# Kernel optimization log

Hardware: AMD Instinct MI355X
Metric: run time of the kernel (lower is better)

Reference implementation:

```python
import jax, jax.numpy as jnp
import numpy as np

T, B, C, HF, H, W, E, TOP_K = 4, 32, 384, 1536, 14, 14, 8, 2
AUX_W = 0.01
ALPHA = 2.0  # spikingjelly ATan surrogate default

@jax.custom_vjp
def spike(v):
    return (v >= 0.0).astype(v.dtype)

def _spike_fwd(v):
    return spike(v), v

def _spike_bwd(v, g):
    sg = (ALPHA / 2.0) / (1.0 + (jnp.pi / 2.0 * ALPHA * v) ** 2)
    return (g * sg,)

spike.defvjp(_spike_fwd, _spike_bwd)

def lif_multistep(x, tau):
    # x: (T, ...). decay_input=True, v_threshold=1, hard reset to 0, detach_reset
    def step(v, xt):
        v = v + (xt - v) / tau
        s = spike(v - 1.0)
        v = v * (1.0 - jax.lax.stop_gradient(s))
        return v, s
    _, s = jax.lax.scan(step, jnp.zeros_like(x[0]), x)
    return s

def bn_eval(y, gamma, beta, mean, var, eps=1e-5):
    inv = gamma / jnp.sqrt(var + eps)
    return y * inv[None, :, None, None] + (beta - mean * inv)[None, :, None, None]

def setup_inputs() -> dict:
    key = jax.random.key(0)
    ks = jax.random.split(key, 8)
    d = {"x": jax.random.normal(ks[0], (T, B, C, H, W), jnp.float32)}
    d["rw"] = jax.random.normal(ks[1], (E, C), jnp.float32) * 0.02
    d["rb"] = jnp.zeros((E,), jnp.float32)
    d["r_gamma"] = jnp.ones((E,), jnp.float32)
    d["r_beta"] = jnp.zeros((E,), jnp.float32)
    d["r_mean"] = jax.random.normal(ks[2], (E,), jnp.float32) * 0.01
    d["r_var"] = jax.random.uniform(ks[3], (E,), jnp.float32, 0.75, 1.25)
    d["w1"] = jax.random.normal(ks[4], (E, HF, C), jnp.float32) * 0.02
    d["b1"] = jnp.zeros((E, HF), jnp.float32)
    d["g1"] = jnp.ones((E, HF), jnp.float32)
    d["be1"] = jnp.zeros((E, HF), jnp.float32)
    d["m1"] = jax.random.normal(ks[5], (E, HF), jnp.float32) * 0.01
    d["v1"] = jnp.ones((E, HF), jnp.float32)
    d["w2"] = jax.random.normal(ks[6], (E, C, HF), jnp.float32) * 0.02
    d["b2"] = jnp.zeros((E, C), jnp.float32)
    d["g2"] = jnp.ones((E, C), jnp.float32)
    d["be2"] = jnp.zeros((E, C), jnp.float32)
    d["m2"] = jax.random.normal(ks[7], (E, C), jnp.float32) * 0.01
    d["v2"] = jnp.ones((E, C), jnp.float32)
    d["taus"] = jnp.linspace(1.5, 4.0, E, dtype=jnp.float32)
    return d

def reference(x, rw, rb, r_gamma, r_beta, r_mean, r_var,
              w1, b1, g1, be1, m1, v1, w2, b2, g2, be2, m2, v2, taus):
    Tn, Bn, Cn, Hn, Wn = x.shape
    N = Tn * Bn
    # ---- SpikeRouter ----
    s = lif_multistep(x, 2.0)                                   # (T,B,C,H,W)
    r = jnp.einsum('tbchw,ec->tbehw', s, rw) + rb[None, None, :, None, None]
    r = bn_eval(r.reshape(N, E, Hn, Wn), r_gamma, r_beta, r_mean, r_var)
    logits = r.mean(axis=(-2, -1))                              # (N,E)
    probs = jax.nn.softmax(logits, axis=-1)
    tkw, tki = jax.lax.top_k(probs, TOP_K)
    tkw = tkw / tkw.sum(axis=-1, keepdims=True)
    one_hot = jax.nn.one_hot(tki, E, dtype=x.dtype)             # (N,K,E)
    gate = (one_hot * tkw[..., None]).sum(axis=1)               # (N,E), 0 for unselected
    # ---- expert dispatch/combine (dense, math-equivalent: gate==0 masks out) ----
    xt = x.reshape(N, Cn, Hn, Wn)
    out = jnp.zeros_like(xt)
    for e in range(E):
        s1 = spike(xt / taus[e] - 1.0)                          # T=1 LIF step
        h = jnp.einsum('nchw,oc->nohw', s1, w1[e]) + b1[e][None, :, None, None]
        h = bn_eval(h, g1[e], be1[e], m1[e], v1[e])
        s2 = spike(h / taus[e] - 1.0)
        o = jnp.einsum('nchw,oc->nohw', s2, w2[e]) + b2[e][None, :, None, None]
        o = bn_eval(o, g2[e], be2[e], m2[e], v2[e])
        o = o + xt                                              # final residual
        out = out + gate[:, e, None, None, None] * o
    # ---- Switch-style load balancing loss ----
    f = one_hot.sum(axis=1).mean(axis=0)                        # fraction routed per expert
    p = probs.mean(axis=0)
    aux = AUX_W * E * jnp.sum(f * p)
    return out.reshape(Tn, Bn, Cn, Hn, Wn), aux
```

## Files before the change

kernel.cpp:

```cpp
#include <hip/hip_runtime.h>
#include <hip/hip_bf16.h>
#include <cstdint>
#include <math.h>

#define T_  4
#define B_  32
#define C_  384
#define HF_ 1536
#define HW_ 196
#define E_  8
#define N_  128
#define REC_CAP 16384
#define NROW 1792
#define NGT  50176
#define LCAP 64

#define LIFB (B_ * C_)
#define TRB  (E_ * 12 * 24)
#define PRB  48

__global__ __launch_bounds__(256) void k_lifprep(
    const float* __restrict__ x, float* __restrict__ cnt,
    const float* __restrict__ w1, __hip_bfloat16* __restrict__ w1t,
    const float* b1, const float* g1, const float* be1,
    const float* m1, const float* v1,
    const float* b2, const float* g2, const float* be2,
    const float* m2, const float* v2,
    const float* taus,
    float* A, float* Bc, float* const2, float* inv2v,
    float* rowmaxp, int* header) {
  __shared__ float tile[64][33];
  __shared__ int c4[T_];
  int blk = blockIdx.x;
  int tid = threadIdx.x;

  if (blk < LIFB) {
    if (tid < T_) c4[tid] = 0;
    __syncthreads();
    int bc = blk;
    bool act = tid < HW_;
    float v = 0.f;
    size_t base = (size_t)bc * HW_ + (act ? tid : 0);
    #pragma unroll
    for (int t = 0; t < T_; ++t) {
      float xv = act ? x[base + (size_t)t * B_ * C_ * HW_] : -1e30f;
      v = v + (xv - v) * 0.5f;
      bool sp = (v - 1.0f >= 0.0f);
      if (sp) v = 0.f;
      unsigned long long m = __ballot(act && sp);
      if ((tid & 63) == 0) atomicAdd(&c4[t], __popcll(m));
    }
    __syncthreads();
    if (tid < T_) cnt[(size_t)tid * B_ * C_ + bc] = (float)c4[tid];
  } else if (blk < LIFB + TRB) {
    int rem = blk - LIFB;
    int e = rem / 288, r2 = rem % 288;
    int ct = r2 / 24, ot = r2 % 24;
    int c0 = ct * 32, o0 = ot * 64;
    int cl = tid & 31, olb = tid >> 5;
    #pragma unroll
    for (int it = 0; it < 8; ++it) {
      int ol = olb + it * 8;
      tile[ol][cl] = w1[(size_t)(e * HF_ + o0 + ol) * C_ + c0 + cl];
    }
    __syncthreads();
    int ol2 = tid & 63, clb = tid >> 6;
    #pragma unroll
    for (int it = 0; it < 8; ++it) {
      int cl2 = clb + it * 4;
      w1t[(size_t)(e * C_ + c0 + cl2) * HF_ + o0 + ol2] =
          __float2bfloat16(tile[ol2][cl2]);
    }
    if (tid < 32) {
      float m = 0.f;
      for (int ol = 0; ol < 64; ++ol) {
        float bv = __bfloat162float(__float2bfloat16(tile[ol][tid]));
        m = fmaxf(m, fabsf(bv));
      }
      rowmaxp[(size_t)(e * C_ + c0 + tid) * 24 + ot] = m;
    }
  } else {
    int idx = (blk - LIFB - TRB) * 256 + tid;
    if (idx < 64) header[idx] = 0;
    if (idx < E_ * HF_) {
      int e = idx / HF_;
      float inv = g1[idx] / sqrtf(v1[idx] + 1e-5f);
      float sh  = be1[idx] - m1[idx] * inv;
      A[idx]  = inv;
      Bc[idx] = inv * b1[idx] + sh - taus[e];
    }
    if (idx < E_ * C_) {
      float inv = g2[idx] / sqrtf(v2[idx] + 1e-5f);
      const2[idx] = b2[idx] * inv + (be2[idx] - m2[idx] * inv);
      inv2v[idx]  = inv;
    }
  }
}

__global__ __launch_bounds__(256) void k_router(
    const float* __restrict__ cnt, const float* __restrict__ rw,
    const float* rb, const float* rg, const float* rbeta,
    const float* rmean, const float* rvar,
    const float* __restrict__ const2,
    const float* __restrict__ rowmaxp, float* __restrict__ rowmax,
    const float* __restrict__ A, const float* __restrict__ Bc,
    float* __restrict__ thrmin,
    int* sel_e, float* sel_g, float* gsum, float* K,
    float* f_acc, float* p_acc) {
  __shared__ float sc[C_ + 256 + E_];
  __shared__ int s_i1, s_i2;
  __shared__ float s_g1, s_g2;
  int bid = blockIdx.x, tid = threadIdx.x;

  if (bid < N_) {
    int n = bid;
    float* part = sc + C_;
    float* lg = part + 256;
    for (int c = tid; c < C_; c += 256) sc[c] = cnt[(size_t)n * C_ + c];
    __syncthreads();
    {
      int e = tid >> 5, sub = tid & 31;
      float d = 0.f;
      for (int c = sub; c < C_; c += 32) d += rw[e * C_ + c] * sc[c];
      part[tid] = d;
    }
    __syncthreads();
    if (tid < E_) {
      float dot = 0.f;
      #pragma unroll
      for (int j = 0; j < 32; ++j) dot += part[tid * 32 + j];
      float inv = rg[tid] / sqrtf(rvar[tid] + 1e-5f);
      lg[tid] = (dot * (1.0f / HW_) + rb[tid]) * inv +
                (rbeta[tid] - rmean[tid] * inv);
    }
    __syncthreads();
    if (tid == 0) {
      float m = lg[0];
      for (int e = 1; e < E_; ++e) m = fmaxf(m, lg[e]);
      float pr[E_]; float s = 0.f;
      for (int e = 0; e < E_; ++e) { pr[e] = expf(lg[e] - m); s += pr[e]; }
      float invs = 1.0f / s;
      for (int e = 0; e < E_; ++e) pr[e] *= invs;
      int i1 = 0;
      for (int e = 1; e < E_; ++e) if (pr[e] > pr[i1]) i1 = e;
      int i2 = (i1 == 0) ? 1 : 0;
      for (int e = 0; e < E_; ++e) if (e != i1 && pr[e] > pr[i2]) i2 = e;
      float w = pr[i1] + pr[i2];
      float ga = pr[i1] / w, gb = pr[i2] / w;
      sel_e[2 * n] = i1; sel_e[2 * n + 1] = i2;
      sel_g[2 * n] = ga; sel_g[2 * n + 1] = gb;
      gsum[n] = ga + gb;
      s_i1 = i1; s_i2 = i2; s_g1 = ga; s_g2 = gb;
      atomicAdd(&f_acc[i1], 1.0f);
      atomicAdd(&f_acc[i2], 1.0f);
      for (int e = 0; e < E_; ++e) atomicAdd(&p_acc[e], pr[e]);
    }
    __syncthreads();
    int i1 = s_i1, i2 = s_i2; float ga = s_g1, gb = s_g2;
    for (int c = tid; c < C_; c += 256)
      K[(size_t)n * C_ + c] =
          ga * const2[i1 * C_ + c] + gb * const2[i2 * C_ + c];
  } else if (bid < N_ + 12) {
    int idx = (bid - N_) * 256 + tid;
    if (idx < E_ * C_) {
      float m = 0.f;
      #pragma unroll
      for (int t = 0; t < 24; ++t) m = fmaxf(m, rowmaxp[(size_t)idx * 24 + t]);
      rowmax[idx] = m;
    }
  } else {
    float* red = sc;
    for (int e = 0; e < E_; ++e) {
      float m = INFINITY;
      for (int o = tid; o < HF_; o += 256) {
        float a = A[e * HF_ + o], b = Bc[e * HF_ + o];
        float thr = (a != 0.0f) ? (-b / fabsf(a))
                                : ((b >= 0.0f) ? -INFINITY : INFINITY);
        m = fminf(m, thr);
      }
      red[tid] = m;
      __syncthreads();
      for (int s = 128; s > 0; s >>= 1) {
        if (tid < s) red[tid] = fminf(red[tid], red[tid + s]);
        __syncthreads();
      }
      if (tid == 0) thrmin[e] = red[0];
      __syncthreads();
    }
  }
}

__global__ __launch_bounds__(256) void k_lists(
    const float* __restrict__ x, const int* __restrict__ sel_e,
    const float* __restrict__ taus, const float* __restrict__ rowmax,
    const float* __restrict__ thrmin,
    const float* __restrict__ gsum, const float* __restrict__ K,
    float* __restrict__ out,
    int* __restrict__ nnzarr, unsigned short* __restrict__ list16) {
  __shared__ float xs[14 * 385];
  int bid = blockIdx.x, tid = threadIdx.x;
  int lane = tid & 63, wave = tid >> 6;
  int n = bid / 14, h = bid - n * 14;
  unsigned long long lmask = (1ull << lane) - 1ull;

  for (int idx = tid; idx < C_ * 7; idx += 256) {
    int c = idx / 7, wp = idx - c * 7;
    float2 v = *(const float2*)(x + ((size_t)(n * C_ + c) * 14 + h) * 14 + 2 * wp);
    xs[(2 * wp) * 385 + c]     = v.x;
    xs[(2 * wp + 1) * 385 + c] = v.y;
  }
  __syncthreads();

  for (int t = wave; t < 28; t += 4) {
    int k = t / 14, w = t - k * 14;
    int pair = 2 * n + k;
    int e = sel_e[pair];
    float tau = taus[e];
    const float* rme = rowmax + e * C_;
    int tw = pair * 196 + h * 14 + w;
    size_t lbase = (size_t)tw * LCAP;
    int nnz = 0;
    float myb = 0.f;
    #pragma unroll
    for (int cb = 0; cb < 6; ++cb) {
      int c = cb * 64 + lane;
      bool sp = (xs[w * 385 + c] / tau - 1.0f >= 0.0f);
      unsigned long long m = __ballot(sp);
      int pos = nnz + __popcll(m & lmask);
      if (sp) {
        if (pos < LCAP) list16[lbase + pos] = (unsigned short)c;
        myb += rme[c];
      }
      nnz += __popcll(m);
    }
    #pragma unroll
    for (int off = 1; off < 64; off <<= 1) myb += __shfl_xor(myb, off, 64);
    if (lane == 0) {
      bool prune = (myb < thrmin[e] - 1e-4f);
      nnzarr[tw] = prune ? -1 : (nnz < LCAP ? nnz : LCAP);
    }
  }

  float g = gsum[n];
  const float* Kn = K + (size_t)n * C_;
  for (int idx = tid; idx < C_ * 7; idx += 256) {
    int c = idx / 7, wp = idx - c * 7;
    float kc = Kn[c];
    float2 v;
    v.x = g * xs[(2 * wp) * 385 + c] + kc;
    v.y = g * xs[(2 * wp + 1) * 385 + c] + kc;
    *(float2*)(out + ((size_t)(n * C_ + c) * 14 + h) * 14 + 2 * wp) = v;
  }
}

__global__ __launch_bounds__(256, 4) void k_gather(
    const __hip_bfloat16* __restrict__ w1t,
    const float* __restrict__ A, const float* __restrict__ Bc,
    const int* __restrict__ sel_e,
    const int* __restrict__ nnzarr, const unsigned short* __restrict__ list16,
    int* __restrict__ rec, int* __restrict__ rec_count) {
  int tw = blockIdx.x * 4 + (threadIdx.x >> 6);
  int lane = threadIdx.x & 63;
  int nnz = nnzarr[tw];
  if (nnz < 0) return;
  int pair = tw / 196, pos = tw - pair * 196;
  int e = sel_e[pair];
  int lv = (int)list16[(size_t)tw * LCAP + lane];
  const uint4* wb = (const uint4*)(w1t + (size_t)e * C_ * HF_);

  #pragma unroll
  for (int pass = 0; pass < 3; ++pass) {
    const uint4* wbp = wb + pass * 64 + lane;
    float acc[8];
    #pragma unroll
    for (int q = 0; q < 8; ++q) acc[q] = 0.f;
    int j = 0;
    for (; j + 4 <= nnz; j += 4) {
      int c0 = __shfl(lv, j + 0);
      int c1 = __shfl(lv, j + 1);
      int c2 = __shfl(lv, j + 2);
      int c3 = __shfl(lv, j + 3);
      uint4 a = wbp[c0 * 192];
      uint4 b = wbp[c1 * 192];
      uint4 c = wbp[c2 * 192];
      uint4 d = wbp[c3 * 192];
      uint32_t ua[4] = {a.x, a.y, a.z, a.w};
      uint32_t ub[4] = {b.x, b.y, b.z, b.w};
      uint32_t uc[4] = {c.x, c.y, c.z, c.w};
      uint32_t ud[4] = {d.x, d.y, d.z, d.w};
      #pragma unroll
      for (int q = 0; q < 4; ++q) {
        acc[2 * q]     += __uint_as_float(ua[q] << 16) + __uint_as_float(ub[q] << 16) +
                          __uint_as_float(uc[q] << 16) + __uint_as_float(ud[q] << 16);
        acc[2 * q + 1] += __uint_as_float(ua[q] & 0xffff0000u) + __uint_as_float(ub[q] & 0xffff0000u) +
                          __uint_as_float(uc[q] & 0xffff0000u) + __uint_as_float(ud[q] & 0xffff0000u);
      }
    }
    for (; j < nnz; ++j) {
      int c0 = __shfl(lv, j);
      uint4 a = wbp[c0 * 192];
      uint32_t ua[4] = {a.x, a.y, a.z, a.w};
      #pragma unroll
      for (int q = 0; q < 4; ++q) {
        acc[2 * q]     += __uint_as_float(ua[q] << 16);
        acc[2 * q + 1] += __uint_as_float(ua[q] & 0xffff0000u);
      }
    }
    int k2 = (pass * 64 + lane) * 2;
    float4 Av0 = ((const float4*)(A + e * HF_))[k2];
    float4 Av1 = ((const float4*)(A + e * HF_))[k2 + 1];
    float4 Bv0 = ((const float4*)(Bc + e * HF_))[k2];
    float4 Bv1 = ((const float4*)(Bc + e * HF_))[k2 + 1];
    float av[8] = {Av0.x, Av0.y, Av0.z, Av0.w, Av1.x, Av1.y, Av1.z, Av1.w};
    float bv[8] = {Bv0.x, Bv0.y, Bv0.z, Bv0.w, Bv1.x, Bv1.y, Bv1.z, Bv1.w};
    #pragma unroll
    for (int q = 0; q < 8; ++q) {
      if (av[q] * acc[q] + bv[q] >= 0.0f) {
        int ridx = atomicAdd(rec_count, 1);
        if (ridx < REC_CAP) {
          rec[ridx * 3 + 0] = pair;
          rec[ridx * 3 + 1] = pos;
          rec[ridx * 3 + 2] = (pass * 64 + lane) * 8 + q;
        }
      }
    }
  }
}

__global__ void k_apply(const int* __restrict__ rec, const int* __restrict__ rec_count,
                        const int* __restrict__ sel_e, const float* __restrict__ sel_g,
                        const float* __restrict__ inv2v, const float* __restrict__ w2,
                        const float* f_acc, const float* p_acc,
                        float* __restrict__ out, float* aux_out) {
  int nrec = *rec_count;
  if (nrec > REC_CAP) nrec = REC_CAP;
  for (int r = blockIdx.x; r < nrec; r += gridDim.x) {
    int pair = rec[r * 3], pos = rec[r * 3 + 1], o = rec[r * 3 + 2];
    int n = pair >> 1;
    int e = sel_e[pair];
    float g = sel_g[pair];
    for (int c = threadIdx.x; c < C_; c += blockDim.x) {
      float wv = w2[(size_t)(e * C_ + c) * HF_ + o];
      atomicAdd(&out[(size_t)(n * C_ + c) * HW_ + pos],
                g * inv2v[e * C_ + c] * wv);
    }
  }
  if (blockIdx.x == 0 && threadIdx.x == 0) {
    float s = 0.f;
    for (int e = 0; e < E_; ++e)
      s += (f_acc[e] * (1.0f / N_)) * (p_acc[e] * (1.0f / N_));
    *aux_out = 0.01f * E_ * s;
  }
}

extern "C" void kernel_launch(void* const* d_in, const int* in_sizes, int n_in,
                              void* d_out, int out_size, void* d_ws, size_t ws_size,
                              hipStream_t stream) {
  const float* x       = (const float*)d_in[0];
  const float* rw      = (const float*)d_in[1];
  const float* rb      = (const float*)d_in[2];
  const float* r_gamma = (const float*)d_in[3];
  const float* r_beta  = (const float*)d_in[4];
  const float* r_mean  = (const float*)d_in[5];
  const float* r_var   = (const float*)d_in[6];
  const float* w1      = (const float*)d_in[7];
  const float* b1      = (const float*)d_in[8];
  const float* g1      = (const float*)d_in[9];
  const float* be1     = (const float*)d_in[10];
  const float* m1      = (const float*)d_in[11];
  const float* v1      = (const float*)d_in[12];
  const float* w2      = (const float*)d_in[13];
  const float* b2      = (const float*)d_in[14];
  const float* g2      = (const float*)d_in[15];
  const float* be2     = (const float*)d_in[16];
  const float* m2      = (const float*)d_in[17];
  const float* v2      = (const float*)d_in[18];
  const float* taus    = (const float*)d_in[19];
  float* out = (float*)d_out;

  char* ws = (char*)d_ws;
  int*   header = (int*)ws;
  float* f_acc  = (float*)ws + 8;
  float* p_acc  = (float*)ws + 16;
  float* cnt    = (float*)(ws + 256);
  int*   sel_e  = (int*)(ws + 196864);
  float* sel_g  = (float*)(ws + 197888);
  float* gsum   = (float*)(ws + 198912);
  float* K      = (float*)(ws + 199424);
  float* A      = (float*)(ws + 396032);
  float* Bc     = (float*)(ws + 445184);
  float* const2 = (float*)(ws + 494336);
  float* inv2v  = (float*)(ws + 506624);
  int*   rec    = (int*)(ws + 518912);
  __hip_bfloat16* w1t = (__hip_bfloat16*)(ws + 715520);
  int*   nnzarr = (int*)(ws + 10152704);
  unsigned short* list16 = (unsigned short*)(ws + 10353408);
  float* rowmaxp = (float*)(ws + 16775936);
  float* rowmax  = (float*)(ws + 17070848);
  float* thrmin  = (float*)(ws + 17083136);

  k_lifprep<<<LIFB + TRB + PRB, 256, 0, stream>>>(
      x, cnt, w1, w1t, b1, g1, be1, m1, v1, b2, g2, be2, m2, v2, taus,
      A, Bc, const2, inv2v, rowmaxp, header);
  k_router<<<N_ + 13, 256, 0, stream>>>(
      cnt, rw, rb, r_gamma, r_beta, r_mean, r_var, const2,
      rowmaxp, rowmax, A, Bc, thrmin,
      sel_e, sel_g, gsum, K, f_acc, p_acc);
  k_lists<<<NROW, 256, 0, stream>>>(
      x, sel_e, taus, rowmax, thrmin, gsum, K, out, nnzarr, list16);
  k_gather<<<NGT / 4, 256, 0, stream>>>(
      w1t, A, Bc, sel_e, nnzarr, list16, rec, header);
  k_apply<<<64, 256, 0, stream>>>(
      rec, header, sel_e, sel_g, inv2v, w2, f_acc, p_acc,
      out, out + (out_size - 1));
}
```

Before: 232.6 us.

## Compact unpruned tokens into a work queue and split combine into its own kernel

The list-building kernel now writes index lists only for positions that survive the pruning test, and appends each survivor to a compact queue through an atomic counter. The gather kernel runs a fixed grid of 2048 blocks as a persistent loop over that queue, so it no longer launches one wave per position only for most to exit early. The dense residual/gate write of the output moves into a separate vectorized float4 kernel. Risks: qcount (header+1) must be zeroed beforehand, presumably in lifprep as for the header. Queue order is nondeterministic, and the extra launch adds overhead.

```diff
diff --git a/kernel.cpp b/kernel.cpp
--- a/kernel.cpp
+++ b/kernel.cpp
@@ -194,9 +194,8 @@
     const float* __restrict__ x, const int* __restrict__ sel_e,
     const float* __restrict__ taus, const float* __restrict__ rowmax,
     const float* __restrict__ thrmin,
-    const float* __restrict__ gsum, const float* __restrict__ K,
-    float* __restrict__ out,
-    int* __restrict__ nnzarr, unsigned short* __restrict__ list16) {
+    unsigned short* __restrict__ list16,
+    int* __restrict__ queue, int* __restrict__ qcount) {
   __shared__ float xs[14 * 385];
   int bid = blockIdx.x, tid = threadIdx.x;
   int lane = tid & 63, wave = tid >> 6;
@@ -217,8 +216,7 @@
     int e = sel_e[pair];
     float tau = taus[e];
     const float* rme = rowmax + e * C_;
-    int tw = pair * 196 + h * 14 + w;
-    size_t lbase = (size_t)tw * LCAP;
+    unsigned long long masks[6];
     int nnz = 0;
     float myb = 0.f;
     #pragma unroll
@@ -226,101 +224,124 @@
       int c = cb * 64 + lane;
       bool sp = (xs[w * 385 + c] / tau - 1.0f >= 0.0f);
       unsigned long long m = __ballot(sp);
-      int pos = nnz + __popcll(m & lmask);
-      if (sp) {
-        if (pos < LCAP) list16[lbase + pos] = (unsigned short)c;
-        myb += rme[c];
-      }
+      masks[cb] = m;
+      if (sp) myb += rme[c];
       nnz += __popcll(m);
     }
     #pragma unroll
     for (int off = 1; off < 64; off <<= 1) myb += __shfl_xor(myb, off, 64);
-    if (lane == 0) {
-      bool prune = (myb < thrmin[e] - 1e-4f);
-      nnzarr[tw] = prune ? -1 : (nnz < LCAP ? nnz : LCAP);
-    }
-  }
-
-  float g = gsum[n];
-  const float* Kn = K + (size_t)n * C_;
-  for (int idx = tid; idx < C_ * 7; idx += 256) {
-    int c = idx / 7, wp = idx - c * 7;
-    float kc = Kn[c];
-    float2 v;
-    v.x = g * xs[(2 * wp) * 385 + c] + kc;
-    v.y = g * xs[(2 * wp + 1) * 385 + c] + kc;
-    *(float2*)(out + ((size_t)(n * C_ + c) * 14 + h) * 14 + 2 * wp) = v;
-  }
+    bool prune = (myb < thrmin[e] - 1e-4f);
+    if (!prune) {
+      int tw = pair * 196 + h * 14 + w;
+      size_t lbase = (size_t)tw * LCAP;
+      int cum = 0;
+      #pragma unroll
+      for (int cb = 0; cb < 6; ++cb) {
+        unsigned long long m = masks[cb];
+        bool sp = (m >> lane) & 1ull;
+        int pos = cum + __popcll(m & lmask);
+        if (sp && pos < LCAP) list16[lbase + pos] = (unsigned short)(cb * 64 + lane);
+        cum += __popcll(m);
+      }
+      if (lane == 0) {
+        int nv = nnz < LCAP ? nnz : LCAP;
+        int qi = atomicAdd(qcount, 1);
+        queue[qi] = tw | (nv << 20);
+      }
+    }
+  }
+}
+
+__global__ __launch_bounds__(256) void k_combine(
+    const float* __restrict__ x, const float* __restrict__ gsum,
+    const float* __restrict__ K, float* __restrict__ out) {
+  int idx = blockIdx.x * 256 + threadIdx.x;
+  int nc = idx / 49;
+  float g = gsum[nc / C_];
+  float kc = K[nc];
+  float4 v = ((const float4*)x)[idx];
+  v.x = g * v.x + kc;
+  v.y = g * v.y + kc;
+  v.z = g * v.z + kc;
+  v.w = g * v.w + kc;
+  ((float4*)out)[idx] = v;
 }
 
 __global__ __launch_bounds__(256, 4) void k_gather(
     const __hip_bfloat16* __restrict__ w1t,
     const float* __restrict__ A, const float* __restrict__ Bc,
     const int* __restrict__ sel_e,
-    const int* __restrict__ nnzarr, const unsigned short* __restrict__ list16,
+    const int* __restrict__ queue, const int* __restrict__ qcount,
+    const unsigned short* __restrict__ list16,
     int* __restrict__ rec, int* __restrict__ rec_count) {
-  int tw = blockIdx.x * 4 + (threadIdx.x >> 6);
+  int nq = *qcount;
+  int wid = blockIdx.x * 4 + (threadIdx.x >> 6);
   int lane = threadIdx.x & 63;
-  int nnz = nnzarr[tw];
-  if (nnz < 0) return;
-  int pair = tw / 196, pos = tw - pair * 196;
-  int e = sel_e[pair];
-  int lv = (int)list16[(size_t)tw * LCAP + lane];
-  const uint4* wb = (const uint4*)(w1t + (size_t)e * C_ * HF_);
-
-  #pragma unroll
-  for (int pass = 0; pass < 3; ++pass) {
-    const uint4* wbp = wb + pass * 64 + lane;
-    float acc[8];
-    #pragma unroll
-    for (int q = 0; q < 8; ++q) acc[q] = 0.f;
-    int j = 0;
-    for (; j + 4 <= nnz; j += 4) {
-      int c0 = __shfl(lv, j + 0);
-      int c1 = __shfl(lv, j + 1);
-      int c2 = __shfl(lv, j + 2);
-      int c3 = __shfl(lv, j + 3);
-      uint4 a = wbp[c0 * 192];
-      uint4 b = wbp[c1 * 192];
-      uint4 c = wbp[c2 * 192];
-      uint4 d = wbp[c3 * 192];
-      uint32_t ua[4] = {a.x, a.y, a.z, a.w};
-      uint32_t ub[4] = {b.x, b.y, b.z, b.w};
-      uint32_t uc[4] = {c.x, c.y, c.z, c.w};
-      uint32_t ud[4] = {d.x, d.y, d.z, d.w};
+  int nwaves = gridDim.x * 4;
+
+  for (int qi = wid; qi < nq; qi += nwaves) {
+    int ent = queue[qi];
+    int tw = ent & 0xFFFFF;
+    int nnz = ent >> 20;
+    int pair = tw / 196, pos = tw - pair * 196;
+    int e = sel_e[pair];
+    int lv = (int)list16[(size_t)tw * LCAP + lane];
+    const uint4* wb = (const uint4*)(w1t + (size_t)e * C_ * HF_);
+
+    #pragma unroll
+    for (int pass = 0; pass < 3; ++pass) {
+      const uint4* wbp = wb + pass * 64 + lane;
+      float acc[8];
       #pragma unroll
-      for (int q = 0; q < 4; ++q) {
-        acc[2 * q]     += __uint_as_float(ua[q] << 16) + __uint_as_float(ub[q] << 16) +
-                          __uint_as_float(uc[q] << 16) + __uint_as_float(ud[q] << 16);
-        acc[2 * q + 1] += __uint_as_float(ua[q] & 0xffff0000u) + __uint_as_float(ub[q] & 0xffff0000u) +
-                          __uint_as_float(uc[q] & 0xffff0000u) + __uint_as_float(ud[q] & 0xffff0000u);
-      }
-    }
-    for (; j < nnz; ++j) {
-      int c0 = __shfl(lv, j);
-      uint4 a = wbp[c0 * 192];
-      uint32_t ua[4] = {a.x, a.y, a.z, a.w};
+      for (int q = 0; q < 8; ++q) acc[q] = 0.f;
+      int j = 0;
+      for (; j + 4 <= nnz; j += 4) {
+        int c0 = __shfl(lv, j + 0);
+        int c1 = __shfl(lv, j + 1);
+        int c2 = __shfl(lv, j + 2);
+        int c3 = __shfl(lv, j + 3);
+        uint4 a = wbp[c0 * 192];
+        uint4 b = wbp[c1 * 192];
+        uint4 c = wbp[c2 * 192];
+        uint4 d = wbp[c3 * 192];
+        uint32_t ua[4] = {a.x, a.y, a.z, a.w};
+        uint32_t ub[4] = {b.x, b.y, b.z, b.w};
+        uint32_t uc[4] = {c.x, c.y, c.z, c.w};
+        uint32_t ud[4] = {d.x, d.y, d.z, d.w};
+        #pragma unroll
+        for (int q = 0; q < 4; ++q) {
+          acc[2 * q]     += __uint_as_float(ua[q] << 16) + __uint_as_float(ub[q] << 16) +
+                            __uint_as_float(uc[q] << 16) + __uint_as_float(ud[q] << 16);
+          acc[2 * q + 1] += __uint_as_float(ua[q] & 0xffff0000u) + __uint_as_float(ub[q] & 0xffff0000u) +
+                            __uint_as_float(uc[q] & 0xffff0000u) + __uint_as_float(ud[q] & 0xffff0000u);
+        }
+      }
+      for (; j < nnz; ++j) {
+        int c0 = __shfl(lv, j);
+        uint4 a = wbp[c0 * 192];
+        uint32_t ua[4] = {a.x, a.y, a.z, a.w};
+        #pragma unroll
+        for (int q = 0; q < 4; ++q) {
+          acc[2 * q]     += __uint_as_float(ua[q] << 16);
+          acc[2 * q + 1] += __uint_as_float(ua[q] & 0xffff0000u);
+        }
+      }
+      int k2 = (pass * 64 + lane) * 2;
+      float4 Av0 = ((const float4*)(A + e * HF_))[k2];
+      float4 Av1 = ((const float4*)(A + e * HF_))[k2 + 1];
+      float4 Bv0 = ((const float4*)(Bc + e * HF_))[k2];
+      float4 Bv1 = ((const float4*)(Bc + e * HF_))[k2 + 1];
+      float av[8] = {Av0.x, Av0.y, Av0.z, Av0.w, Av1.x, Av1.y, Av1.z, Av1.w};
+      float bv[8] = {Bv0.x, Bv0.y, Bv0.z, Bv0.w, Bv1.x, Bv1.y, Bv1.z, Bv1.w};
       #pragma unroll
-      for (int q = 0; q < 4; ++q) {
-        acc[2 * q]     += __uint_as_float(ua[q] << 16);
-        acc[2 * q + 1] += __uint_as_float(ua[q] & 0xffff0000u);
-      }
-    }
-    int k2 = (pass * 64 + lane) * 2;
-    float4 Av0 = ((const float4*)(A + e * HF_))[k2];
-    float4 Av1 = ((const float4*)(A + e * HF_))[k2 + 1];
-    float4 Bv0 = ((const float4*)(Bc + e * HF_))[k2];
-    float4 Bv1 = ((const float4*)(Bc + e * HF_))[k2 + 1];
-    float av[8] = {Av0.x, Av0.y, Av0.z, Av0.w, Av1.x, Av1.y, Av1.z, Av1.w};
-    float bv[8] = {Bv0.x, Bv0.y, Bv0.z, Bv0.w, Bv1.x, Bv1.y, Bv1.z, Bv1.w};
-    #pragma unroll
-    for (int q = 0; q < 8; ++q) {
-      if (av[q] * acc[q] + bv[q] >= 0.0f) {
-        int ridx = atomicAdd(rec_count, 1);
-        if (ridx < REC_CAP) {
-          rec[ridx * 3 + 0] = pair;
-          rec[ridx * 3 + 1] = pos;
-          rec[ridx * 3 + 2] = (pass * 64 + lane) * 8 + q;
+      for (int q = 0; q < 8; ++q) {
+        if (av[q] * acc[q] + bv[q] >= 0.0f) {
+          int ridx = atomicAdd(rec_count, 1);
+          if (ridx < REC_CAP) {
+            rec[ridx * 3 + 0] = pair;
+            rec[ridx * 3 + 1] = pos;
+            rec[ridx * 3 + 2] = (pass * 64 + lane) * 8 + q;
+          }
         }
       }
     }
@@ -393,11 +414,12 @@
   float* inv2v  = (float*)(ws + 506624);
   int*   rec    = (int*)(ws + 518912);
   __hip_bfloat16* w1t = (__hip_bfloat16*)(ws + 715520);
-  int*   nnzarr = (int*)(ws + 10152704);
+  int*   queue  = (int*)(ws + 10152704);
   unsigned short* list16 = (unsigned short*)(ws + 10353408);
   float* rowmaxp = (float*)(ws + 16775936);
   float* rowmax  = (float*)(ws + 17070848);
   float* thrmin  = (float*)(ws + 17083136);
+  int* qcount = header + 1;
 
   k_lifprep<<<LIFB + TRB + PRB, 256, 0, stream>>>(
       x, cnt, w1, w1t, b1, g1, be1, m1, v1, b2, g2, be2, m2, v2, taus,
@@ -407,9 +429,10 @@
       rowmaxp, rowmax, A, Bc, thrmin,
       sel_e, sel_g, gsum, K, f_acc, p_acc);
   k_lists<<<NROW, 256, 0, stream>>>(
-      x, sel_e, taus, rowmax, thrmin, gsum, K, out, nnzarr, list16);
-  k_gather<<<NGT / 4, 256, 0, stream>>>(
-      w1t, A, Bc, sel_e, nnzarr, list16, rec, header);
+      x, sel_e, taus, rowmax, thrmin, list16, queue, qcount);
+  k_combine<<<(N_ * C_ * 49) / 256, 256, 0, stream>>>(x, gsum, K, out);
+  k_gather<<<2048, 256, 0, stream>>>(
+      w1t, A, Bc, sel_e, queue, qcount, list16, rec, header);
   k_apply<<<64, 256, 0, stream>>>(
       rec, header, sel_e, sel_g, inv2v, w2, f_acc, p_acc,
       out, out + (out_size - 1));
```

Result: faster. 219.9 us (-5.4%).
